# Kernel tuning notes

Hardware: AMD Instinct MI355X
Metric: run time of the kernel (lower is better)

## Reference

```python
import jax, jax.numpy as jnp
import numpy as np

EMBED_DIM = 1024
NUM_HEADS = 16
HEAD_DIM = EMBED_DIM // NUM_HEADS


def setup_inputs() -> dict:
    key = jax.random.key(0)
    k1, k2, k3, k4 = jax.random.split(key, 4)
    scale = 1.0 / np.sqrt(EMBED_DIM)
    x = jax.random.normal(k1, (2, 2048, EMBED_DIM), dtype=jnp.float32)
    Wqkv = jax.random.normal(k2, (3 * EMBED_DIM, EMBED_DIM), dtype=jnp.float32) * scale
    Wproj = jax.random.normal(k3, (EMBED_DIM, EMBED_DIM), dtype=jnp.float32) * scale
    bproj = jax.random.normal(k4, (EMBED_DIM,), dtype=jnp.float32) * 0.01
    return {"x": x, "Wqkv": Wqkv, "Wproj": Wproj, "bproj": bproj}


def reference(x, Wqkv, Wproj, bproj):
    B, T, D = x.shape
    # QKV projection (torch Linear: x @ W.T), no bias
    qkv = jnp.einsum('btd,ed->bte', x, Wqkv)              # [B, T, 3D]
    qkv = qkv.reshape(B, T, 3, NUM_HEADS, HEAD_DIM)
    qkv = jnp.transpose(qkv, (2, 0, 3, 1, 4))             # [3, B, H, T, hd]
    q, k, v = qkv[0], qkv[1], qkv[2]
    # scaled dot-product attention (full matrix, as in source)
    dots = jnp.einsum('bhqd,bhkd->bhqk', q, k) / jnp.sqrt(jnp.asarray(HEAD_DIM, x.dtype))
    attn = jax.nn.softmax(dots, axis=-1)
    out = jnp.einsum('bhqk,bhkd->bhqd', attn, v)          # [B, H, T, hd]
    out = jnp.transpose(out, (0, 2, 1, 3)).reshape(B, T, D)
    # output projection with bias
    return jnp.einsum('btd,ed->bte', out, Wproj) + bproj
```

## Files before the change

kernel.cpp:

```cpp
#include <hip/hip_runtime.h>

typedef __attribute__((ext_vector_type(8))) short bf16x8;
typedef __attribute__((ext_vector_type(4))) short bf16x4;
typedef __attribute__((ext_vector_type(4))) float f32x4;
typedef __attribute__((ext_vector_type(2))) unsigned int u32x2;

#define MFMA32(a, b, c) __builtin_amdgcn_mfma_f32_16x16x32_bf16((a), (b), (c), 0, 0, 0)
#define MFMA16K(a, b, c) __builtin_amdgcn_mfma_f32_16x16x16bf16_1k((a), (b), (c), 0, 0, 0)

__device__ __forceinline__ unsigned short f2bf(float f) {
    unsigned u = __builtin_bit_cast(unsigned, f);
    u = (u + 0x7fffu + ((u >> 16) & 1u)) >> 16;
    return (unsigned short)u;
}

__device__ __forceinline__ unsigned cvtpk(float lo, float hi) {
    unsigned r;
    asm("v_cvt_pk_bf16_f32 %0, %1, %2" : "=v"(r) : "v"(lo), "v"(hi));
    return r;
}

__device__ __forceinline__ void gll16(const void* g, void* l) {
    __builtin_amdgcn_global_load_lds((__attribute__((address_space(1))) void*)g,
                                     (__attribute__((address_space(3))) void*)l,
                                     16, 0, 0);
}

__global__ __launch_bounds__(256) void castall(const float* __restrict__ x,
                                               const float* __restrict__ wqkv,
                                               const float* __restrict__ wproj,
                                               unsigned short* __restrict__ xb,
                                               unsigned short* __restrict__ wqkvb,
                                               unsigned short* __restrict__ wprojb) {
    const int N0 = 1048576, N1 = 786432, N2 = 262144;
    int stride = gridDim.x * blockDim.x;
    for (int i = blockIdx.x * blockDim.x + threadIdx.x; i < N0 + N1 + N2; i += stride) {
        const float4* s;
        ushort4* d;
        int k;
        if (i < N0) { s = (const float4*)x; d = (ushort4*)xb; k = i; }
        else if (i < N0 + N1) { s = (const float4*)wqkv; d = (ushort4*)wqkvb; k = i - N0; }
        else { s = (const float4*)wproj; d = (ushort4*)wprojb; k = i - N0 - N1; }
        float4 v = s[k];
        ushort4 o;
        o.x = f2bf(v.x); o.y = f2bf(v.y); o.z = f2bf(v.z); o.w = f2bf(v.w);
        d[k] = o;
    }
}

template <int EPI, int TN>
__global__ __launch_bounds__(256) void gemm_bt(const unsigned short* __restrict__ A,
                                               const unsigned short* __restrict__ B,
                                               int K,
                                               unsigned short* __restrict__ qbuf,
                                               unsigned short* __restrict__ kbuf,
                                               unsigned short* __restrict__ vtb,
                                               float* __restrict__ outF,
                                               const float* __restrict__ bias) {
    __shared__ __align__(16) unsigned short As[2][4096];
    __shared__ __align__(16) unsigned short Bs[2][TN * 32];
    const int tid = threadIdx.x;
    const int w = tid >> 6, l = tid & 63;
    const int g = l >> 4, cc = l & 15;
    constexpr int MI = (TN == 128) ? 4 : 2;
    const int wr = (TN == 128) ? (w >> 1) : w;
    const int wc = (TN == 128) ? (w & 1) : 0;

    const int nwg = gridDim.x * gridDim.y;
    const int lin = blockIdx.y * gridDim.x + blockIdx.x;
    const int swz = (lin & 7) * (nwg >> 3) + (lin >> 3);
    const int bx = swz % gridDim.x, by = swz / gridDim.x;
    const int m0 = by * 128, n0 = bx * TN;

    f32x4 acc[MI][4];
#pragma unroll
    for (int i = 0; i < MI; ++i)
#pragma unroll
        for (int j = 0; j < 4; ++j) acc[i][j] = (f32x4){0.f, 0.f, 0.f, 0.f};

    const int srow = (l >> 2);
    const int skk = (l & 3) * 8;

#define GSTAGE(bb, k0)                                                              \
    do {                                                                            \
        _Pragma("unroll") for (int ch = 0; ch < 2; ++ch) {                          \
            int ci = ch * 4 + w;                                                    \
            gll16(A + (size_t)(m0 + ci * 16 + srow) * K + (k0) + skk,               \
                  &As[bb][ci * 512]);                                               \
        }                                                                           \
        if constexpr (TN == 128) {                                                  \
            _Pragma("unroll") for (int ch = 0; ch < 2; ++ch) {                      \
                int ci = ch * 4 + w;                                                \
                gll16(B + (size_t)(n0 + ci * 16 + srow) * K + (k0) + skk,           \
                      &Bs[bb][ci * 512]);                                           \
            }                                                                       \
        } else {                                                                    \
            gll16(B + (size_t)(n0 + w * 16 + srow) * K + (k0) + skk,                \
                  &Bs[bb][w * 512]);                                                \
        }                                                                           \
    } while (0)

    GSTAGE(0, 0);
    asm volatile("s_waitcnt vmcnt(0)" ::: "memory");
    __syncthreads();

    const int nt = K >> 5;
    int cur = 0;
    for (int t = 0; t < nt; ++t) {
        if (t + 1 < nt) GSTAGE(cur ^ 1, (t + 1) * 32);
        bf16x8 af[MI], bfr[4];
#pragma unroll
        for (int i = 0; i < MI; ++i)
            af[i] = *(const bf16x8*)&As[cur][(wr * (MI * 16) + i * 16 + cc) * 32 + g * 8];
#pragma unroll
        for (int j = 0; j < 4; ++j)
            bfr[j] = *(const bf16x8*)&Bs[cur][(wc * 64 + j * 16 + cc) * 32 + g * 8];
        __builtin_amdgcn_s_setprio(1);
#pragma unroll
        for (int i = 0; i < MI; ++i)
#pragma unroll
            for (int j = 0; j < 4; ++j) acc[i][j] = MFMA32(af[i], bfr[j], acc[i][j]);
        __builtin_amdgcn_s_setprio(0);
        asm volatile("s_waitcnt vmcnt(0)" ::: "memory");
        __syncthreads();
        cur ^= 1;
    }
#undef GSTAGE

    if (EPI == 0) {
        const int which = n0 >> 10;
#pragma unroll
        for (int jn = 0; jn < 4; ++jn) {
            int n = n0 + wc * 64 + jn * 16 + cc;
            int hn = n & 1023;
            int h = hn >> 6, d = hn & 63;
#pragma unroll
            for (int i = 0; i < MI; ++i) {
#pragma unroll
                for (int j = 0; j < 4; ++j) {
                    int m = m0 + wr * (MI * 16) + i * 16 + g * 4 + j;
                    int b = m >> 11, t = m & 2047;
                    int bh = b * 16 + h;
                    float v = acc[i][jn][j];
                    if (which == 0) {
                        qbuf[((size_t)bh * 2048 + t) * 64 + d] = f2bf(v * 0.1803368801f);
                    } else if (which == 1) {
                        kbuf[((size_t)bh * 2048 + t) * 64 + d] = f2bf(v);
                    } else {
                        vtb[((size_t)bh * 64 + d) * 2048 + t] = f2bf(v);
                    }
                }
            }
        }
    } else {
#pragma unroll
        for (int jn = 0; jn < 4; ++jn) {
            int n = n0 + wc * 64 + jn * 16 + cc;
            float bn = bias[n];
#pragma unroll
            for (int i = 0; i < MI; ++i) {
#pragma unroll
                for (int j = 0; j < 4; ++j) {
                    int m = m0 + wr * (MI * 16) + i * 16 + g * 4 + j;
                    outF[(size_t)m * 1024 + n] = acc[i][jn][j] + bn;
                }
            }
        }
    }
}

__global__ __launch_bounds__(256) void attn_kernel(const unsigned short* __restrict__ qb,
                                                   const unsigned short* __restrict__ kb,
                                                   const unsigned short* __restrict__ vtb,
                                                   unsigned short* __restrict__ ao) {
    __shared__ __align__(16) unsigned short smem[16384];
    const int bh = blockIdx.y;
    const int w = threadIdx.x >> 6, l = threadIdx.x & 63;
    const int g = l >> 4, cc = l & 15;
    const int q0 = blockIdx.x * 128 + w * 32;

    const unsigned short* qbase = qb + (size_t)bh * 2048 * 64;
    const unsigned short* kbase = kb + (size_t)bh * 2048 * 64;
    const unsigned short* vbase = vtb + (size_t)bh * 64 * 2048;

    const int sl8 = l >> 3, sl7 = l & 7;
    const int sperm = ((sl7 ^ sl8) * 8);

#define STAGE(bb, kk)                                                                        \
    do {                                                                                     \
        int base = (bb) * 8192;                                                              \
        gll16(kbase + (size_t)((kk) + w * 8 + sl8) * 64 + sperm, &smem[base + w * 512]);     \
        gll16(kbase + (size_t)((kk) + (w + 4) * 8 + sl8) * 64 + sperm,                       \
              &smem[base + (w + 4) * 512]);                                                  \
        gll16(vbase + (size_t)(w * 8 + sl8) * 2048 + (kk) + sperm,                           \
              &smem[base + 4096 + w * 512]);                                                 \
        gll16(vbase + (size_t)((w + 4) * 8 + sl8) * 2048 + (kk) + sperm,                     \
              &smem[base + 4096 + (w + 4) * 512]);                                           \
    } while (0)

    bf16x8 qf[2][2];
#pragma unroll
    for (int qt = 0; qt < 2; ++qt)
#pragma unroll
        for (int kh = 0; kh < 2; ++kh)
            qf[qt][kh] = *(const bf16x8*)(qbase + (size_t)(q0 + qt * 16 + cc) * 64 + kh * 32 + g * 8);

    float lrun[2] = {0.f, 0.f};
    f32x4 acc[2][4];
#pragma unroll
    for (int qt = 0; qt < 2; ++qt)
#pragma unroll
        for (int dt = 0; dt < 4; ++dt) acc[qt][dt] = (f32x4){0.f, 0.f, 0.f, 0.f};

    const int swz = cc & 7;

    STAGE(0, 0);
    asm volatile("s_waitcnt vmcnt(0)" ::: "memory");
    __syncthreads();

    for (int t = 0; t < 32; ++t) {
        const int cb = t & 1;
        if (t + 1 < 32) STAGE(cb ^ 1, (t + 1) * 64);

        const unsigned short* Kb = &smem[cb * 8192];
        const unsigned short* Vb = Kb + 4096;

        bf16x8 kf[4][2];
#pragma unroll
        for (int kt = 0; kt < 4; ++kt)
#pragma unroll
            for (int kh = 0; kh < 2; ++kh)
                kf[kt][kh] = *(const bf16x8*)&Kb[(kt * 16 + cc) * 64 + (((kh * 4 + g) ^ swz) * 8)];

        f32x4 s[2][4];
        __builtin_amdgcn_s_setprio(1);
#pragma unroll
        for (int qt = 0; qt < 2; ++qt)
#pragma unroll
            for (int kt = 0; kt < 4; ++kt) {
                f32x4 z = (f32x4){0.f, 0.f, 0.f, 0.f};
                z = MFMA32(kf[kt][0], qf[qt][0], z);
                z = MFMA32(kf[kt][1], qf[qt][1], z);
                s[qt][kt] = z;
            }
        __builtin_amdgcn_s_setprio(0);

        bf16x4 pf[2][4];
#pragma unroll
        for (int qt = 0; qt < 2; ++qt) {
#pragma unroll
            for (int kt = 0; kt < 4; ++kt) {
                float p0 = __builtin_amdgcn_exp2f(s[qt][kt][0]);
                float p1 = __builtin_amdgcn_exp2f(s[qt][kt][1]);
                float p2 = __builtin_amdgcn_exp2f(s[qt][kt][2]);
                float p3 = __builtin_amdgcn_exp2f(s[qt][kt][3]);
                lrun[qt] += (p0 + p1) + (p2 + p3);
                u32x2 wv;
                wv.x = cvtpk(p0, p1);
                wv.y = cvtpk(p2, p3);
                pf[qt][kt] = __builtin_bit_cast(bf16x4, wv);
            }
        }

        __builtin_amdgcn_s_setprio(1);
#pragma unroll
        for (int kt = 0; kt < 4; ++kt) {
            const int seg = ((kt * 2 + (g >> 1)) ^ swz);
#pragma unroll
            for (int dt = 0; dt < 4; ++dt) {
                bf16x4 vf = *(const bf16x4*)&Vb[(dt * 16 + cc) * 64 + seg * 8 + (g & 1) * 4];
                acc[0][dt] = MFMA16K(vf, pf[0][kt], acc[0][dt]);
                acc[1][dt] = MFMA16K(vf, pf[1][kt], acc[1][dt]);
            }
        }
        __builtin_amdgcn_s_setprio(0);

        asm volatile("s_waitcnt vmcnt(0)" ::: "memory");
        __syncthreads();
    }
#undef STAGE

    const int b = bh >> 4, h = bh & 15;
#pragma unroll
    for (int qt = 0; qt < 2; ++qt) {
        float lsum = lrun[qt];
        lsum += __shfl_xor(lsum, 16);
        lsum += __shfl_xor(lsum, 32);
        float inv = 1.f / lsum;
        size_t rowbase = ((size_t)(b * 2048 + q0 + qt * 16 + cc)) * 1024 + h * 64;
#pragma unroll
        for (int dt = 0; dt < 4; ++dt) {
            u32x2 ov;
            ov.x = cvtpk(acc[qt][dt][0] * inv, acc[qt][dt][1] * inv);
            ov.y = cvtpk(acc[qt][dt][2] * inv, acc[qt][dt][3] * inv);
            *(u32x2*)(ao + rowbase + dt * 16 + g * 4) = ov;
        }
    }
}

extern "C" void kernel_launch(void* const* d_in, const int* in_sizes, int n_in,
                              void* d_out, int out_size, void* d_ws, size_t ws_size,
                              hipStream_t stream) {
    const float* x = (const float*)d_in[0];
    const float* Wqkv = (const float*)d_in[1];
    const float* Wproj = (const float*)d_in[2];
    const float* bproj = (const float*)d_in[3];
    float* out = (float*)d_out;

    unsigned short* xb = (unsigned short*)d_ws;
    unsigned short* wqkvb = xb + 4096 * 1024;
    unsigned short* wprojb = wqkvb + 3072 * 1024;
    unsigned short* qbuf = wprojb + 1024 * 1024;
    unsigned short* kbuf = qbuf + 32 * 2048 * 64;
    unsigned short* vtb = kbuf + 32 * 2048 * 64;
    unsigned short* aob = vtb + 32 * 2048 * 64;

    castall<<<2048, 256, 0, stream>>>(x, Wqkv, Wproj, xb, wqkvb, wprojb);

    gemm_bt<0, 128><<<dim3(24, 32), 256, 0, stream>>>(xb, wqkvb, 1024, qbuf, kbuf, vtb, nullptr, nullptr);
    attn_kernel<<<dim3(16, 32), 256, 0, stream>>>(qbuf, kbuf, vtb, aob);
    gemm_bt<1, 64><<<dim3(16, 32), 256, 0, stream>>>(aob, wprojb, 1024, nullptr, nullptr, nullptr, out, bproj);
}
```

Baseline: 196.8 us.

## Split attention KV range across two wave groups and swizzle GEMM LDS tiles

The attention kernel now launches 512 threads per block. Two groups of four waves each process half of the 2048 keys into separate LDS double buffers. Their partial accumulators and row sums are then merged through LDS before normalization and the bf16 store. This doubles the resident waves per block to hide latency, at the cost of twice the LDS footprint, an extra barrier and a combine step. Separately, the GEMM applies an XOR swizzle to the global-to-LDS staging column and the matching fragment reads, to reduce LDS bank conflicts.

```diff
diff --git a/kernel.cpp b/kernel.cpp
--- a/kernel.cpp
+++ b/kernel.cpp
@@ -79,7 +79,8 @@
         for (int j = 0; j < 4; ++j) acc[i][j] = (f32x4){0.f, 0.f, 0.f, 0.f};
 
     const int srow = (l >> 2);
-    const int skk = (l & 3) * 8;
+    const int skk = ((l & 3) ^ ((l >> 3) & 3)) * 8;
+    const int gsw = (g ^ ((cc >> 1) & 3)) * 8;
 
 #define GSTAGE(bb, k0)                                                              \
     do {                                                                            \
@@ -111,10 +112,10 @@
         bf16x8 af[MI], bfr[4];
 #pragma unroll
         for (int i = 0; i < MI; ++i)
-            af[i] = *(const bf16x8*)&As[cur][(wr * (MI * 16) + i * 16 + cc) * 32 + g * 8];
+            af[i] = *(const bf16x8*)&As[cur][(wr * (MI * 16) + i * 16 + cc) * 32 + gsw];
 #pragma unroll
         for (int j = 0; j < 4; ++j)
-            bfr[j] = *(const bf16x8*)&Bs[cur][(wc * 64 + j * 16 + cc) * 32 + g * 8];
+            bfr[j] = *(const bf16x8*)&Bs[cur][(wc * 64 + j * 16 + cc) * 32 + gsw];
         __builtin_amdgcn_s_setprio(1);
 #pragma unroll
         for (int i = 0; i < MI; ++i)
@@ -169,15 +170,17 @@
     }
 }
 
-__global__ __launch_bounds__(256) void attn_kernel(const unsigned short* __restrict__ qb,
-                                                   const unsigned short* __restrict__ kb,
-                                                   const unsigned short* __restrict__ vtb,
-                                                   unsigned short* __restrict__ ao) {
-    __shared__ __align__(16) unsigned short smem[16384];
+__global__ __launch_bounds__(512, 4) void attn_kernel(const unsigned short* __restrict__ qb,
+                                                      const unsigned short* __restrict__ kb,
+                                                      const unsigned short* __restrict__ vtb,
+                                                      unsigned short* __restrict__ ao) {
+    __shared__ __align__(16) unsigned short smem[32768];
     const int bh = blockIdx.y;
     const int w = threadIdx.x >> 6, l = threadIdx.x & 63;
     const int g = l >> 4, cc = l & 15;
-    const int q0 = blockIdx.x * 128 + w * 32;
+    const int grp = w >> 2, wq = w & 3;
+    const int q0 = blockIdx.x * 128 + wq * 32;
+    const int kvoff = grp * 1024;
 
     const unsigned short* qbase = qb + (size_t)bh * 2048 * 64;
     const unsigned short* kbase = kb + (size_t)bh * 2048 * 64;
@@ -186,16 +189,16 @@
     const int sl8 = l >> 3, sl7 = l & 7;
     const int sperm = ((sl7 ^ sl8) * 8);
 
-#define STAGE(bb, kk)                                                                        \
-    do {                                                                                     \
-        int base = (bb) * 8192;                                                              \
-        gll16(kbase + (size_t)((kk) + w * 8 + sl8) * 64 + sperm, &smem[base + w * 512]);     \
-        gll16(kbase + (size_t)((kk) + (w + 4) * 8 + sl8) * 64 + sperm,                       \
-              &smem[base + (w + 4) * 512]);                                                  \
-        gll16(vbase + (size_t)(w * 8 + sl8) * 2048 + (kk) + sperm,                           \
-              &smem[base + 4096 + w * 512]);                                                 \
-        gll16(vbase + (size_t)((w + 4) * 8 + sl8) * 2048 + (kk) + sperm,                     \
-              &smem[base + 4096 + (w + 4) * 512]);                                           \
+#define STAGE(bb, kk)                                                                          \
+    do {                                                                                       \
+        int base = grp * 16384 + (bb) * 8192;                                                  \
+        gll16(kbase + (size_t)((kk) + wq * 8 + sl8) * 64 + sperm, &smem[base + wq * 512]);     \
+        gll16(kbase + (size_t)((kk) + (wq + 4) * 8 + sl8) * 64 + sperm,                        \
+              &smem[base + (wq + 4) * 512]);                                                   \
+        gll16(vbase + (size_t)(wq * 8 + sl8) * 2048 + (kk) + sperm,                            \
+              &smem[base + 4096 + wq * 512]);                                                  \
+        gll16(vbase + (size_t)((wq + 4) * 8 + sl8) * 2048 + (kk) + sperm,                      \
+              &smem[base + 4096 + (wq + 4) * 512]);                                            \
     } while (0)
 
     bf16x8 qf[2][2];
@@ -214,15 +217,15 @@
 
     const int swz = cc & 7;
 
-    STAGE(0, 0);
+    STAGE(0, kvoff);
     asm volatile("s_waitcnt vmcnt(0)" ::: "memory");
     __syncthreads();
 
-    for (int t = 0; t < 32; ++t) {
+    for (int t = 0; t < 16; ++t) {
         const int cb = t & 1;
-        if (t + 1 < 32) STAGE(cb ^ 1, (t + 1) * 64);
-
-        const unsigned short* Kb = &smem[cb * 8192];
+        if (t + 1 < 16) STAGE(cb ^ 1, kvoff + (t + 1) * 64);
+
+        const unsigned short* Kb = &smem[grp * 16384 + cb * 8192];
         const unsigned short* Vb = Kb + 4096;
 
         bf16x8 kf[4][2];
@@ -280,20 +283,45 @@
     }
 #undef STAGE
 
-    const int b = bh >> 4, h = bh & 15;
+    float lsum[2];
 #pragma unroll
     for (int qt = 0; qt < 2; ++qt) {
-        float lsum = lrun[qt];
-        lsum += __shfl_xor(lsum, 16);
-        lsum += __shfl_xor(lsum, 32);
-        float inv = 1.f / lsum;
-        size_t rowbase = ((size_t)(b * 2048 + q0 + qt * 16 + cc)) * 1024 + h * 64;
-#pragma unroll
-        for (int dt = 0; dt < 4; ++dt) {
-            u32x2 ov;
-            ov.x = cvtpk(acc[qt][dt][0] * inv, acc[qt][dt][1] * inv);
-            ov.y = cvtpk(acc[qt][dt][2] * inv, acc[qt][dt][3] * inv);
-            *(u32x2*)(ao + rowbase + dt * 16 + g * 4) = ov;
+        float v = lrun[qt];
+        v += __shfl_xor(v, 16);
+        v += __shfl_xor(v, 32);
+        lsum[qt] = v;
+    }
+
+    float* cs = (float*)smem;
+    const int slot = (wq * 64 + l) * 35;
+    if (grp == 1) {
+#pragma unroll
+        for (int qt = 0; qt < 2; ++qt)
+#pragma unroll
+            for (int dt = 0; dt < 4; ++dt)
+#pragma unroll
+                for (int j = 0; j < 4; ++j) cs[slot + (qt * 4 + dt) * 4 + j] = acc[qt][dt][j];
+        cs[slot + 32] = lsum[0];
+        cs[slot + 33] = lsum[1];
+    }
+    __syncthreads();
+    if (grp == 0) {
+        const int b = bh >> 4, h = bh & 15;
+#pragma unroll
+        for (int qt = 0; qt < 2; ++qt) {
+            float inv = 1.f / (lsum[qt] + cs[slot + 32 + qt]);
+            size_t rowbase = ((size_t)(b * 2048 + q0 + qt * 16 + cc)) * 1024 + h * 64;
+#pragma unroll
+            for (int dt = 0; dt < 4; ++dt) {
+                float r0 = acc[qt][dt][0] + cs[slot + (qt * 4 + dt) * 4 + 0];
+                float r1 = acc[qt][dt][1] + cs[slot + (qt * 4 + dt) * 4 + 1];
+                float r2 = acc[qt][dt][2] + cs[slot + (qt * 4 + dt) * 4 + 2];
+                float r3 = acc[qt][dt][3] + cs[slot + (qt * 4 + dt) * 4 + 3];
+                u32x2 ov;
+                ov.x = cvtpk(r0 * inv, r1 * inv);
+                ov.y = cvtpk(r2 * inv, r3 * inv);
+                *(u32x2*)(ao + rowbase + dt * 16 + g * 4) = ov;
+            }
         }
     }
 }
@@ -318,6 +346,6 @@
     castall<<<2048, 256, 0, stream>>>(x, Wqkv, Wproj, xb, wqkvb, wprojb);
 
     gemm_bt<0, 128><<<dim3(24, 32), 256, 0, stream>>>(xb, wqkvb, 1024, qbuf, kbuf, vtb, nullptr, nullptr);
-    attn_kernel<<<dim3(16, 32), 256, 0, stream>>>(qbuf, kbuf, vtb, aob);
+    attn_kernel<<<dim3(16, 32), 512, 0, stream>>>(qbuf, kbuf, vtb, aob);
     gemm_bt<1, 64><<<dim3(16, 32), 256, 0, stream>>>(aob, wprojb, 1024, nullptr, nullptr, nullptr, out, bproj);
 }
```

Result: faster. 186.4 us (-5.3%).
